# Optimization experiments

Measured on AMD Instinct MI355X. Metric: run time of the kernel, lower is better.

The kernel has to match this reference:

```python
import jax, jax.numpy as jnp
import numpy as np

NUM_HEADS = 16
HIDDEN = 1024
HEAD_DIM = HIDDEN // NUM_HEADS
B, L = 2, 2048


def setup_inputs() -> dict:
    key = jax.random.key(0)
    ks = jax.random.split(key, 5)
    scale = 1.0 / np.sqrt(HIDDEN)
    return {
        "x": jax.random.normal(ks[0], (B, L, HIDDEN), dtype=jnp.float32),
        "Wq": jax.random.normal(ks[1], (HIDDEN, HIDDEN), dtype=jnp.float32) * scale,
        "Wk": jax.random.normal(ks[2], (HIDDEN, HIDDEN), dtype=jnp.float32) * scale,
        "Wv": jax.random.normal(ks[3], (HIDDEN, HIDDEN), dtype=jnp.float32) * scale,
        "Wo": jax.random.normal(ks[4], (HIDDEN, HIDDEN), dtype=jnp.float32) * scale,
    }


def reference(x, Wq, Wk, Wv, Wo):
    b, l, _ = x.shape
    # projections (torch nn.Linear: y = x @ W.T), reshape to (B,L,H,D)
    q = (x @ Wq.T).reshape(b, l, NUM_HEADS, HEAD_DIM)
    k = (x @ Wk.T).reshape(b, l, NUM_HEADS, HEAD_DIM)
    v = (x @ Wv.T).reshape(b, l, NUM_HEADS, HEAD_DIM)
    # positive feature map
    q = jax.nn.elu(q) + 1.0
    k = jax.nn.elu(k) + 1.0
    # causal linear attention via cumulative kv outer products
    kv = jnp.einsum('blhd,blhe->blhde', k, v)          # (B,L,H,D,D)
    kv_cumsum = jnp.cumsum(kv, axis=1)
    k_cumsum = jnp.cumsum(k, axis=1)
    out = jnp.einsum('blhd,blhde->blhe', q, kv_cumsum)  # (B,L,H,D)
    normalizer = jnp.clip(jnp.einsum('blhd,blhd->blh', q, k_cumsum), 1e-6, None)
    out = out / normalizer[..., None]
    out = out.reshape(b, l, HIDDEN)
    return out @ Wo.T
```

## Files before the change

### kernel.cpp

```cpp
#include <hip/hip_runtime.h>
#include <cstdint>
#include <cstddef>

#define HID 1024
#define NH 16
#define HD 64
#define BB 2
#define LL 2048
#define MM (BB*LL)
#define CHUNK 64
#define NT (LL/CHUNK)
#define BHn (BB*NH)
#define SP 72

typedef __bf16 bf16;
typedef __attribute__((ext_vector_type(8))) __bf16 bf16x8;
typedef __attribute__((ext_vector_type(4))) float f32x4;

__device__ __forceinline__ f32x4 mfma16(bf16x8 a, bf16x8 b, f32x4 c){
  return __builtin_amdgcn_mfma_f32_16x16x32_bf16(a, b, c, 0, 0, 0);
}

__device__ __forceinline__ void gload16(const void* g, void* l){
  __builtin_amdgcn_global_load_lds(
      (const __attribute__((address_space(1))) unsigned int*)g,
      (__attribute__((address_space(3))) unsigned int*)l, 16, 0, 0);
}

__device__ __forceinline__ void barx(){
  asm volatile("" ::: "memory");
  __builtin_amdgcn_s_barrier();
  asm volatile("" ::: "memory");
}

#define WAITVM(N) asm volatile("s_waitcnt vmcnt(" #N ")" ::: "memory")

__global__ __launch_bounds__(256) void cast_all_k(
    const float* __restrict__ x,  const float* __restrict__ w0,
    const float* __restrict__ w1, const float* __restrict__ w2, const float* __restrict__ w3,
    bf16* __restrict__ xb, bf16* __restrict__ d0, bf16* __restrict__ d1,
    bf16* __restrict__ d2, bf16* __restrict__ d3)
{
  int bid = blockIdx.x;
  const float* s; bf16* d; int base;
  if (bid < 2048){ s = x; d = xb; base = bid; }
  else {
    int w = (bid - 2048) >> 9, r = (bid - 2048) & 511;
    s = (w==0)?w0:(w==1)?w1:(w==2)?w2:w3;
    d = (w==0)?d0:(w==1)?d1:(w==2)?d2:d3;
    base = r;
  }
  size_t i = (size_t)(base*256 + threadIdx.x) * 8;
  float4 v0 = *(const float4*)(s + i);
  float4 v1 = *(const float4*)(s + i + 4);
  union { bf16 h[8]; uint4 u; } pk;
  pk.h[0]=(bf16)v0.x; pk.h[1]=(bf16)v0.y; pk.h[2]=(bf16)v0.z; pk.h[3]=(bf16)v0.w;
  pk.h[4]=(bf16)v1.x; pk.h[5]=(bf16)v1.y; pk.h[6]=(bf16)v1.z; pk.h[7]=(bf16)v1.w;
  *(uint4*)(d + i) = pk.u;
}

template<int MODE>
__global__ __launch_bounds__(512, 2) void gemm8_k(
    const bf16* __restrict__ A,
    const bf16* __restrict__ W0, const bf16* __restrict__ W1, const bf16* __restrict__ W2,
    bf16* __restrict__ Qo, bf16* __restrict__ Kn, bf16* __restrict__ Vn,
    float* __restrict__ Outf)
{
  constexpr int NKT = HID/32;
  __shared__ bf16 lds[4][2][128*32];

  const int tid = threadIdx.x;
  const int wv = tid >> 6, lane = tid & 63;
  const int lrow = lane & 15, g4 = lane >> 4;
  const int wr = wv >> 2, wc = wv & 3;
  int bn = blockIdx.x, wsel = 0;
  const bf16* W = W0;
  if (MODE==0){ wsel = bn >> 3; bn &= 7; W = (wsel==0)?W0:((wsel==1)?W1:W2); }
  const int row0 = blockIdx.y*128, col0 = bn*128;

  const int sr = tid >> 2, sc = tid & 3;
  const int scs = sc ^ ((sr>>1)&3);
  const bf16* gA = A + (size_t)(row0 + sr)*HID + scs*8;
  const bf16* gB = W + (size_t)(col0 + sr)*HID + scs*8;
  const int ldst = tid*8;

  auto stage_tile = [&](int u){
    const int buf = u & 3;
    gload16(gA + u*32, (void*)&lds[buf][0][ldst]);
    gload16(gB + u*32, (void*)&lds[buf][1][ldst]);
  };

  const int koff = (g4 ^ ((lrow>>1)&3)) << 3;

  auto read_frags = [&](int u, bf16x8 (&fa)[4], bf16x8 (&fb)[2]){
    const int buf = u & 3;
    #pragma unroll
    for (int i=0;i<4;i++)
      fa[i] = *(const bf16x8*)&lds[buf][0][((wr*64 + i*16+lrow)<<5) + koff];
    #pragma unroll
    for (int j=0;j<2;j++)
      fb[j] = *(const bf16x8*)&lds[buf][1][((wc*32 + j*16+lrow)<<5) + koff];
  };

  f32x4 acc[4][2] = {};
  auto do_mfma = [&](bf16x8 (&fa)[4], bf16x8 (&fb)[2]){
    __builtin_amdgcn_s_setprio(1);
    #pragma unroll
    for (int i=0;i<4;i++)
      #pragma unroll
      for (int j=0;j<2;j++)
        acc[i][j] = mfma16(fa[i], fb[j], acc[i][j]);
    __builtin_amdgcn_s_setprio(0);
  };

  stage_tile(0); stage_tile(1); stage_tile(2);
  WAITVM(4);
  barx();
  bf16x8 fEa[4], fEb[2], fOa[4], fOb[2];
  read_frags(0, fEa, fEb);

  for (int t=0; t<NKT; t+=2){
    if (t+3 < NKT)      { stage_tile(t+3); WAITVM(4); }
    else if (t+3 == NKT){ WAITVM(2); }
    else                { WAITVM(0); }
    barx();
    read_frags(t+1, fOa, fOb);
    do_mfma(fEa, fEb);
    const int t2 = t+1;
    if (t2 < NKT-1){
      if (t2+3 < NKT)      { stage_tile(t2+3); WAITVM(4); }
      else if (t2+3 == NKT){ WAITVM(2); }
      else                 { WAITVM(0); }
      barx();
      read_frags(t2+1, fEa, fEb);
    }
    do_mfma(fOa, fOb);
  }

  #pragma unroll
  for (int i=0;i<4;i++){
    const int m0 = row0 + wr*64 + i*16 + g4*4;
    #pragma unroll
    for (int j=0;j<2;j++){
      const int c = col0 + wc*32 + j*16 + lrow;
      #pragma unroll
      for (int r=0;r<4;r++){
        float v = acc[i][j][r];
        if (MODE==1){
          Outf[(size_t)(m0+r)*HID + c] = v;
        } else {
          if (wsel<2) v = v>0.f ? v+1.f : __expf(v);
          bf16 bv = (bf16)v;
          if      (wsel==0) Qo[(size_t)(m0+r)*HID + c] = bv;
          else if (wsel==1) Kn[(size_t)(m0+r)*HID + c] = bv;
          else              Vn[(size_t)(m0+r)*HID + c] = bv;
        }
      }
    }
  }
}

__global__ __launch_bounds__(256) void pass1_k(const bf16* __restrict__ Kn, const bf16* __restrict__ Vn,
                                               float* __restrict__ SkvT, float* __restrict__ ksum)
{
  __shared__ bf16 KT[64*SP];
  __shared__ bf16 VT[64*SP];
  const int blk = blockIdx.x;
  const int bh = blk >> 5, t = blk & (NT-1);
  const int b = bh>>4, h = bh&15;
  const int tid = threadIdx.x;
  const int we = tid >> 6, lane = tid & 63;
  const int lrow = lane&15, g4 = lane>>4, lk8 = g4*8;
  const int sj = tid >> 2, c4 = tid & 3;
  const bf16* kb = Kn + ((size_t)(b*LL + t*CHUNK))*HID + h*HD;
  const bf16* vb = Vn + ((size_t)(b*LL + t*CHUNK))*HID + h*HD;

  {
    const bf16* ks = kb + (size_t)sj*HID + c4*16;
    const bf16* vs = vb + (size_t)sj*HID + c4*16;
    bf16x8 kr0 = *(const bf16x8*)&ks[0], kr1 = *(const bf16x8*)&ks[8];
    bf16x8 vr0 = *(const bf16x8*)&vs[0], vr1 = *(const bf16x8*)&vs[8];
    #pragma unroll
    for (int e=0;e<8;e++){
      KT[(c4*16+e)*SP + sj]   = kr0[e];
      KT[(c4*16+8+e)*SP + sj] = kr1[e];
      VT[(c4*16+e)*SP + sj]   = vr0[e];
      VT[(c4*16+8+e)*SP + sj] = vr1[e];
    }
  }
  __syncthreads();

  f32x4 acc[4] = {};
  #pragma unroll
  for (int kk=0;kk<2;kk++){
    bf16x8 fa = *(const bf16x8*)&VT[(we*16 + lrow)*SP + kk*32 + lk8];
    #pragma unroll
    for (int j=0;j<4;j++){
      bf16x8 fb = *(const bf16x8*)&KT[(j*16 + lrow)*SP + kk*32 + lk8];
      acc[j] = mfma16(fa, fb, acc[j]);
    }
  }
  float* so = SkvT + (size_t)blk*4096;
  #pragma unroll
  for (int j=0;j<4;j++)
    #pragma unroll
    for (int r=0;r<4;r++)
      so[(we*16 + g4*4 + r)*64 + j*16 + lrow] = acc[j][r];

  {
    const int row = we*16 + lrow;
    float s = 0.f;
    #pragma unroll
    for (int u=0;u<2;u++){
      bf16x8 k8 = *(const bf16x8*)&KT[row*SP + g4*16 + u*8];
      #pragma unroll
      for (int e=0;e<8;e++) s += (float)k8[e];
    }
    s += __shfl_xor(s,16); s += __shfl_xor(s,32);
    if (g4==0) ksum[(size_t)blk*64 + row] = s;
  }
}

__global__ __launch_bounds__(256) void pass2_k(const float* __restrict__ SkvT, const float* __restrict__ ksum,
                                               bf16* __restrict__ Sexcl, float* __restrict__ ksx)
{
  int gid = blockIdx.x*256 + threadIdx.x;
  if (gid < BHn*4096){
    int bh = gid >> 12, e = gid & 4095;
    float run = 0.f;
    size_t base = (size_t)bh*NT*4096 + e;
    #pragma unroll 4
    for (int t=0;t<NT;t++){
      Sexcl[base + (size_t)t*4096] = (bf16)run;
      run += SkvT[base + (size_t)t*4096];
    }
  } else if (gid < BHn*4096 + BHn*64){
    int g2 = gid - BHn*4096;
    int bh = g2 >> 6, d = g2 & 63;
    float run = 0.f;
    size_t base = (size_t)bh*NT*64 + d;
    #pragma unroll 4
    for (int t=0;t<NT;t++){
      ksx[base + (size_t)t*64] = run;
      run += ksum[base + (size_t)t*64];
    }
  }
}

__global__ __launch_bounds__(256) void pass3_k(const bf16* __restrict__ Q, const bf16* __restrict__ Kn,
                                               const bf16* __restrict__ Sexcl, const bf16* __restrict__ Vn,
                                               const float* __restrict__ ksx, bf16* __restrict__ Obuf)
{
  __shared__ bf16 P[64*SP];
  __shared__ bf16 VT[64*SP];
  const int blk = blockIdx.x;
  const int bh = blk>>5, t = blk&(NT-1);
  const int b = bh>>4, h = bh&15;
  const int tid = threadIdx.x;
  const int w = tid>>6, lane = tid&63;
  const int lrow = lane&15, g4 = lane>>4, lk8 = g4*8;
  const int sj = tid>>2, c4 = tid&3;
  const bf16* qb = Q  + ((size_t)(b*LL + t*CHUNK))*HID + h*HD;
  const bf16* kb = Kn + ((size_t)(b*LL + t*CHUNK))*HID + h*HD;
  const bf16* vb = Vn + ((size_t)(b*LL + t*CHUNK))*HID + h*HD;

  {
    const bf16* vs = vb + (size_t)sj*HID + c4*16;
    bf16x8 vr0 = *(const bf16x8*)&vs[0], vr1 = *(const bf16x8*)&vs[8];
    #pragma unroll
    for (int e=0;e<8;e++){
      VT[(c4*16+e)*SP + sj]   = vr0[e];
      VT[(c4*16+8+e)*SP + sj] = vr1[e];
    }
  }

  bf16x8 aq[2], bk[4][2];
  #pragma unroll
  for (int kk=0;kk<2;kk++){
    aq[kk] = *(const bf16x8*)&qb[(size_t)(w*16+lrow)*HID + kk*32 + lk8];
    #pragma unroll
    for (int j=0;j<4;j++)
      bk[j][kk] = *(const bf16x8*)&kb[(size_t)(j*16+lrow)*HID + kk*32 + lk8];
  }
  f32x4 sacc[4] = {};
  #pragma unroll
  for (int kk=0;kk<2;kk++)
    #pragma unroll
    for (int j=0;j<4;j++)
      sacc[j] = mfma16(aq[kk], bk[j][kk], sacc[j]);
  float rs[4];
  #pragma unroll
  for (int r=0;r<4;r++){
    int irow = w*16 + g4*4 + r;
    float p = 0.f;
    #pragma unroll
    for (int j=0;j<4;j++){
      int jcol = j*16 + lrow;
      float v = (jcol <= irow) ? sacc[j][r] : 0.f;
      sacc[j][r] = v;
      p += v;
    }
    p += __shfl_xor(p,1); p += __shfl_xor(p,2);
    p += __shfl_xor(p,4); p += __shfl_xor(p,8);
    rs[r] = p;
  }
  #pragma unroll
  for (int j=0;j<4;j++)
    #pragma unroll
    for (int r=0;r<4;r++)
      P[(w*16+g4*4+r)*SP + j*16+lrow] = (bf16)sacc[j][r];
  const float* kp = ksx + (size_t)blk*64;
  float zA;
  {
    float s = 0.f;
    #pragma unroll
    for (int kk=0;kk<2;kk++){
      const float* k8 = kp + kk*32 + lk8;
      bf16x8 q = aq[kk];
      #pragma unroll
      for (int j=0;j<8;j++) s += (float)q[j] * k8[j];
    }
    s += __shfl_xor(s,16); s += __shfl_xor(s,32);
    zA = s;
  }
  const bf16* sb = Sexcl + (size_t)blk*4096;
  f32x4 oacc[4] = {};
  #pragma unroll
  for (int kk=0;kk<2;kk++)
    #pragma unroll
    for (int j=0;j<4;j++){
      bf16x8 bs = *(const bf16x8*)&sb[(size_t)(j*16+lrow)*64 + kk*32 + lk8];
      oacc[j] = mfma16(aq[kk], bs, oacc[j]);
    }
  __syncthreads();
  #pragma unroll
  for (int kk=0;kk<2;kk++){
    bf16x8 ap = *(const bf16x8*)&P[(w*16+lrow)*SP + kk*32 + lk8];
    #pragma unroll
    for (int j=0;j<4;j++){
      bf16x8 bv = *(const bf16x8*)&VT[(j*16+lrow)*SP + kk*32 + lk8];
      oacc[j] = mfma16(ap, bv, oacc[j]);
    }
  }
  bf16* ob = Obuf + ((size_t)(b*LL + t*CHUNK))*HID + h*HD;
  #pragma unroll
  for (int r=0;r<4;r++){
    float z = __shfl(zA, g4*4 + r) + rs[r];
    z = fmaxf(z, 1e-6f);
    float inv = 1.0f/z;
    int irow = w*16 + g4*4 + r;
    #pragma unroll
    for (int j=0;j<4;j++)
      ob[(size_t)irow*HID + j*16+lrow] = (bf16)(oacc[j][r]*inv);
  }
}

extern "C" void kernel_launch(void* const* d_in, const int* in_sizes, int n_in,
                              void* d_out, int out_size, void* d_ws, size_t ws_size,
                              hipStream_t stream)
{
  const float* x  = (const float*)d_in[0];
  const float* Wq = (const float*)d_in[1];
  const float* Wk = (const float*)d_in[2];
  const float* Wv = (const float*)d_in[3];
  const float* Wo = (const float*)d_in[4];
  float* out = (float*)d_out;

  char* p = (char*)d_ws;
  auto alloc = [&](size_t bytes){ void* r = (void*)p; p += (bytes + 255) & ~(size_t)255; return r; };
  bf16* xb   = (bf16*)alloc((size_t)MM*HID*2);
  bf16* Wqb  = (bf16*)alloc((size_t)HID*HID*2);
  bf16* Wkb  = (bf16*)alloc((size_t)HID*HID*2);
  bf16* Wvb  = (bf16*)alloc((size_t)HID*HID*2);
  bf16* Wob  = (bf16*)alloc((size_t)HID*HID*2);
  bf16* Qb   = (bf16*)alloc((size_t)MM*HID*2);
  bf16* Knb  = (bf16*)alloc((size_t)MM*HID*2);
  bf16* Vnb  = (bf16*)alloc((size_t)MM*HID*2);
  bf16* Ob   = (bf16*)alloc((size_t)MM*HID*2);
  float* SkvT  = (float*)alloc((size_t)BHn*NT*4096*4);
  bf16*  Sexcl = (bf16*) alloc((size_t)BHn*NT*4096*2);
  float* ksum  = (float*)alloc((size_t)BHn*NT*64*4);
  float* ksx   = (float*)alloc((size_t)BHn*NT*64*4);

  cast_all_k<<<dim3(4096), 256, 0, stream>>>(x, Wq,Wk,Wv,Wo, xb, Wqb,Wkb,Wvb,Wob);
  gemm8_k<0><<<dim3(24,32), 512, 0, stream>>>(xb, Wqb,Wkb,Wvb, Qb,Knb,Vnb, nullptr);
  pass1_k<<<dim3(BHn*NT), 256, 0, stream>>>(Knb, Vnb, SkvT, ksum);
  pass2_k<<<dim3((BHn*4096 + BHn*64 + 255)/256), 256, 0, stream>>>(SkvT, ksum, Sexcl, ksx);
  pass3_k<<<dim3(BHn*NT), 256, 0, stream>>>(Qb, Knb, Sexcl, Vnb, ksx, Ob);
  gemm8_k<1><<<dim3(8,32), 512, 0, stream>>>(Ob, Wob,nullptr,nullptr, nullptr,nullptr,nullptr, out);
}
```

Baseline: 156.7 us.

## Group chunk pairs into segments for linear-attention state scan

Each block now handles a segment of two 64-row chunks instead of one. The per-segment KV state is summed in segsum, scanned over 16 segments rather than 32, and the attention kernel updates the running state inside the block between its two chunks. This halves the number of state matrices written, scanned and read through global memory. In exchange there are half as many blocks, serial work inside each block, and an extra bf16 rounding of the in-block state update.

```diff
diff --git a/kernel.cpp b/kernel.cpp
--- a/kernel.cpp
+++ b/kernel.cpp
@@ -10,6 +10,7 @@
 #define MM (BB*LL)
 #define CHUNK 64
 #define NT (LL/CHUNK)
+#define NSEG 16
 #define BHn (BB*NH)
 #define SP 72
 
@@ -160,198 +161,259 @@
   }
 }
 
-__global__ __launch_bounds__(256) void pass1_k(const bf16* __restrict__ Kn, const bf16* __restrict__ Vn,
-                                               float* __restrict__ SkvT, float* __restrict__ ksum)
+__global__ __launch_bounds__(256, 2) void segsum_k(const bf16* __restrict__ Kn, const bf16* __restrict__ Vn,
+                                                   float* __restrict__ Sseg, float* __restrict__ kseg)
 {
   __shared__ bf16 KT[64*SP];
   __shared__ bf16 VT[64*SP];
-  const int blk = blockIdx.x;
-  const int bh = blk >> 5, t = blk & (NT-1);
+  const int bx = blockIdx.x;
+  const int bh = bx >> 4, seg = bx & (NSEG-1);
   const int b = bh>>4, h = bh&15;
   const int tid = threadIdx.x;
   const int we = tid >> 6, lane = tid & 63;
   const int lrow = lane&15, g4 = lane>>4, lk8 = g4*8;
   const int sj = tid >> 2, c4 = tid & 3;
-  const bf16* kb = Kn + ((size_t)(b*LL + t*CHUNK))*HID + h*HD;
-  const bf16* vb = Vn + ((size_t)(b*LL + t*CHUNK))*HID + h*HD;
-
-  {
-    const bf16* ks = kb + (size_t)sj*HID + c4*16;
-    const bf16* vs = vb + (size_t)sj*HID + c4*16;
-    bf16x8 kr0 = *(const bf16x8*)&ks[0], kr1 = *(const bf16x8*)&ks[8];
-    bf16x8 vr0 = *(const bf16x8*)&vs[0], vr1 = *(const bf16x8*)&vs[8];
-    #pragma unroll
-    for (int e=0;e<8;e++){
-      KT[(c4*16+e)*SP + sj]   = kr0[e];
-      KT[(c4*16+8+e)*SP + sj] = kr1[e];
-      VT[(c4*16+e)*SP + sj]   = vr0[e];
-      VT[(c4*16+8+e)*SP + sj] = vr1[e];
-    }
-  }
-  __syncthreads();
 
   f32x4 acc[4] = {};
+  float krow = 0.f;
+
   #pragma unroll
-  for (int kk=0;kk<2;kk++){
-    bf16x8 fa = *(const bf16x8*)&VT[(we*16 + lrow)*SP + kk*32 + lk8];
-    #pragma unroll
-    for (int j=0;j<4;j++){
-      bf16x8 fb = *(const bf16x8*)&KT[(j*16 + lrow)*SP + kk*32 + lk8];
-      acc[j] = mfma16(fa, fb, acc[j]);
-    }
-  }
-  float* so = SkvT + (size_t)blk*4096;
+  for (int c=0;c<2;c++){
+    const int cg = seg*2 + c;
+    const bf16* kb = Kn + ((size_t)(b*LL + cg*CHUNK))*HID + h*HD;
+    const bf16* vb = Vn + ((size_t)(b*LL + cg*CHUNK))*HID + h*HD;
+    {
+      const bf16* ks = kb + (size_t)sj*HID + c4*16;
+      const bf16* vs = vb + (size_t)sj*HID + c4*16;
+      bf16x8 kr0 = *(const bf16x8*)&ks[0], kr1 = *(const bf16x8*)&ks[8];
+      bf16x8 vr0 = *(const bf16x8*)&vs[0], vr1 = *(const bf16x8*)&vs[8];
+      #pragma unroll
+      for (int e=0;e<8;e++){
+        KT[(c4*16+e)*SP + sj]   = kr0[e];
+        KT[(c4*16+8+e)*SP + sj] = kr1[e];
+        VT[(c4*16+e)*SP + sj]   = vr0[e];
+        VT[(c4*16+8+e)*SP + sj] = vr1[e];
+      }
+    }
+    __syncthreads();
+    #pragma unroll
+    for (int kk=0;kk<2;kk++){
+      bf16x8 fa = *(const bf16x8*)&VT[(we*16 + lrow)*SP + kk*32 + lk8];
+      #pragma unroll
+      for (int j=0;j<4;j++){
+        bf16x8 fb = *(const bf16x8*)&KT[(j*16 + lrow)*SP + kk*32 + lk8];
+        acc[j] = mfma16(fa, fb, acc[j]);
+      }
+    }
+    {
+      const int row = we*16 + lrow;
+      float s = 0.f;
+      #pragma unroll
+      for (int u=0;u<2;u++){
+        bf16x8 k8 = *(const bf16x8*)&KT[row*SP + g4*16 + u*8];
+        #pragma unroll
+        for (int e=0;e<8;e++) s += (float)k8[e];
+      }
+      s += __shfl_xor(s,16); s += __shfl_xor(s,32);
+      krow += s;
+    }
+    __syncthreads();
+  }
+
+  float* so = Sseg + (size_t)bx*4096;
   #pragma unroll
   for (int j=0;j<4;j++)
     #pragma unroll
     for (int r=0;r<4;r++)
       so[(we*16 + g4*4 + r)*64 + j*16 + lrow] = acc[j][r];
-
-  {
-    const int row = we*16 + lrow;
-    float s = 0.f;
-    #pragma unroll
-    for (int u=0;u<2;u++){
-      bf16x8 k8 = *(const bf16x8*)&KT[row*SP + g4*16 + u*8];
-      #pragma unroll
-      for (int e=0;e<8;e++) s += (float)k8[e];
-    }
-    s += __shfl_xor(s,16); s += __shfl_xor(s,32);
-    if (g4==0) ksum[(size_t)blk*64 + row] = s;
-  }
-}
-
-__global__ __launch_bounds__(256) void pass2_k(const float* __restrict__ SkvT, const float* __restrict__ ksum,
-                                               bf16* __restrict__ Sexcl, float* __restrict__ ksx)
+  if (g4==0) kseg[(size_t)bx*64 + we*16 + lrow] = krow;
+}
+
+__global__ __launch_bounds__(256) void segscan_k(const float* __restrict__ Sseg, const float* __restrict__ kseg,
+                                                 bf16* __restrict__ Sexb, float* __restrict__ ksxb)
 {
   int gid = blockIdx.x*256 + threadIdx.x;
   if (gid < BHn*4096){
     int bh = gid >> 12, e = gid & 4095;
     float run = 0.f;
-    size_t base = (size_t)bh*NT*4096 + e;
+    size_t base = (size_t)bh*NSEG*4096 + e;
     #pragma unroll 4
-    for (int t=0;t<NT;t++){
-      Sexcl[base + (size_t)t*4096] = (bf16)run;
-      run += SkvT[base + (size_t)t*4096];
+    for (int s=0;s<NSEG;s++){
+      Sexb[base + (size_t)s*4096] = (bf16)run;
+      run += Sseg[base + (size_t)s*4096];
     }
   } else if (gid < BHn*4096 + BHn*64){
     int g2 = gid - BHn*4096;
     int bh = g2 >> 6, d = g2 & 63;
     float run = 0.f;
-    size_t base = (size_t)bh*NT*64 + d;
+    size_t base = (size_t)bh*NSEG*64 + d;
     #pragma unroll 4
-    for (int t=0;t<NT;t++){
-      ksx[base + (size_t)t*64] = run;
-      run += ksum[base + (size_t)t*64];
-    }
-  }
-}
-
-__global__ __launch_bounds__(256) void pass3_k(const bf16* __restrict__ Q, const bf16* __restrict__ Kn,
-                                               const bf16* __restrict__ Sexcl, const bf16* __restrict__ Vn,
-                                               const float* __restrict__ ksx, bf16* __restrict__ Obuf)
-{
-  __shared__ bf16 P[64*SP];
+    for (int s=0;s<NSEG;s++){
+      ksxb[base + (size_t)s*64] = run;
+      run += kseg[base + (size_t)s*64];
+    }
+  }
+}
+
+__global__ __launch_bounds__(256, 2) void attn_k(const bf16* __restrict__ Q, const bf16* __restrict__ Kn,
+                                                 const bf16* __restrict__ Vn, const bf16* __restrict__ Sexb,
+                                                 const float* __restrict__ ksxb, bf16* __restrict__ Obuf)
+{
+  __shared__ bf16 KT[64*SP];
   __shared__ bf16 VT[64*SP];
-  const int blk = blockIdx.x;
-  const int bh = blk>>5, t = blk&(NT-1);
+  __shared__ bf16 P [64*SP];
+  __shared__ bf16 Sm[64*SP];
+  __shared__ float ksum_lds[64];
+  const int bx = blockIdx.x;
+  const int bh = bx >> 4, seg = bx & (NSEG-1);
   const int b = bh>>4, h = bh&15;
   const int tid = threadIdx.x;
-  const int w = tid>>6, lane = tid&63;
+  const int w = tid >> 6, lane = tid & 63;
   const int lrow = lane&15, g4 = lane>>4, lk8 = g4*8;
-  const int sj = tid>>2, c4 = tid&3;
-  const bf16* qb = Q  + ((size_t)(b*LL + t*CHUNK))*HID + h*HD;
-  const bf16* kb = Kn + ((size_t)(b*LL + t*CHUNK))*HID + h*HD;
-  const bf16* vb = Vn + ((size_t)(b*LL + t*CHUNK))*HID + h*HD;
-
+  const int sj = tid >> 2, c4 = tid & 3;
+
+  if (tid < 64) ksum_lds[tid] = ksxb[(size_t)bx*64 + tid];
   {
-    const bf16* vs = vb + (size_t)sj*HID + c4*16;
-    bf16x8 vr0 = *(const bf16x8*)&vs[0], vr1 = *(const bf16x8*)&vs[8];
-    #pragma unroll
-    for (int e=0;e<8;e++){
-      VT[(c4*16+e)*SP + sj]   = vr0[e];
-      VT[(c4*16+8+e)*SP + sj] = vr1[e];
-    }
-  }
-
-  bf16x8 aq[2], bk[4][2];
-  #pragma unroll
-  for (int kk=0;kk<2;kk++){
-    aq[kk] = *(const bf16x8*)&qb[(size_t)(w*16+lrow)*HID + kk*32 + lk8];
-    #pragma unroll
-    for (int j=0;j<4;j++)
-      bk[j][kk] = *(const bf16x8*)&kb[(size_t)(j*16+lrow)*HID + kk*32 + lk8];
-  }
-  f32x4 sacc[4] = {};
-  #pragma unroll
-  for (int kk=0;kk<2;kk++)
-    #pragma unroll
-    for (int j=0;j<4;j++)
-      sacc[j] = mfma16(aq[kk], bk[j][kk], sacc[j]);
-  float rs[4];
-  #pragma unroll
-  for (int r=0;r<4;r++){
-    int irow = w*16 + g4*4 + r;
-    float p = 0.f;
-    #pragma unroll
-    for (int j=0;j<4;j++){
-      int jcol = j*16 + lrow;
-      float v = (jcol <= irow) ? sacc[j][r] : 0.f;
-      sacc[j][r] = v;
-      p += v;
-    }
-    p += __shfl_xor(p,1); p += __shfl_xor(p,2);
-    p += __shfl_xor(p,4); p += __shfl_xor(p,8);
-    rs[r] = p;
-  }
+    const bf16* sp = Sexb + (size_t)bx*4096 + tid*16;
+    bf16x8 s0 = *(const bf16x8*)&sp[0], s1 = *(const bf16x8*)&sp[8];
+    const int e = tid>>2, d0 = (tid&3)*16;
+    *(bf16x8*)&Sm[e*SP + d0]     = s0;
+    *(bf16x8*)&Sm[e*SP + d0 + 8] = s1;
+  }
+  __syncthreads();
+  f32x4 Srun[4];
   #pragma unroll
   for (int j=0;j<4;j++)
     #pragma unroll
     for (int r=0;r<4;r++)
-      P[(w*16+g4*4+r)*SP + j*16+lrow] = (bf16)sacc[j][r];
-  const float* kp = ksx + (size_t)blk*64;
-  float zA;
-  {
-    float s = 0.f;
+      Srun[j][r] = (float)Sm[(w*16+g4*4+r)*SP + j*16+lrow];
+
+  #pragma unroll
+  for (int c=0;c<2;c++){
+    const int cg = seg*2 + c;
+    const bf16* kb = Kn + ((size_t)(b*LL + cg*CHUNK))*HID + h*HD;
+    const bf16* vb = Vn + ((size_t)(b*LL + cg*CHUNK))*HID + h*HD;
+    const bf16* qb = Q  + ((size_t)(b*LL + cg*CHUNK))*HID + h*HD;
+    {
+      const bf16* ks = kb + (size_t)sj*HID + c4*16;
+      const bf16* vs = vb + (size_t)sj*HID + c4*16;
+      bf16x8 kr0 = *(const bf16x8*)&ks[0], kr1 = *(const bf16x8*)&ks[8];
+      bf16x8 vr0 = *(const bf16x8*)&vs[0], vr1 = *(const bf16x8*)&vs[8];
+      #pragma unroll
+      for (int e=0;e<8;e++){
+        KT[(c4*16+e)*SP + sj]   = kr0[e];
+        KT[(c4*16+8+e)*SP + sj] = kr1[e];
+        VT[(c4*16+e)*SP + sj]   = vr0[e];
+        VT[(c4*16+8+e)*SP + sj] = vr1[e];
+      }
+    }
+    bf16x8 aq[2], bk[4][2];
     #pragma unroll
     for (int kk=0;kk<2;kk++){
-      const float* k8 = kp + kk*32 + lk8;
-      bf16x8 q = aq[kk];
-      #pragma unroll
-      for (int j=0;j<8;j++) s += (float)q[j] * k8[j];
-    }
-    s += __shfl_xor(s,16); s += __shfl_xor(s,32);
-    zA = s;
-  }
-  const bf16* sb = Sexcl + (size_t)blk*4096;
-  f32x4 oacc[4] = {};
-  #pragma unroll
-  for (int kk=0;kk<2;kk++)
-    #pragma unroll
-    for (int j=0;j<4;j++){
-      bf16x8 bs = *(const bf16x8*)&sb[(size_t)(j*16+lrow)*64 + kk*32 + lk8];
-      oacc[j] = mfma16(aq[kk], bs, oacc[j]);
-    }
-  __syncthreads();
-  #pragma unroll
-  for (int kk=0;kk<2;kk++){
-    bf16x8 ap = *(const bf16x8*)&P[(w*16+lrow)*SP + kk*32 + lk8];
-    #pragma unroll
-    for (int j=0;j<4;j++){
-      bf16x8 bv = *(const bf16x8*)&VT[(j*16+lrow)*SP + kk*32 + lk8];
-      oacc[j] = mfma16(ap, bv, oacc[j]);
-    }
-  }
-  bf16* ob = Obuf + ((size_t)(b*LL + t*CHUNK))*HID + h*HD;
-  #pragma unroll
-  for (int r=0;r<4;r++){
-    float z = __shfl(zA, g4*4 + r) + rs[r];
-    z = fmaxf(z, 1e-6f);
-    float inv = 1.0f/z;
-    int irow = w*16 + g4*4 + r;
+      aq[kk] = *(const bf16x8*)&qb[(size_t)(w*16+lrow)*HID + kk*32 + lk8];
+      #pragma unroll
+      for (int j=0;j<4;j++)
+        bk[j][kk] = *(const bf16x8*)&kb[(size_t)(j*16+lrow)*HID + kk*32 + lk8];
+    }
+    __syncthreads();
+    f32x4 sacc[4] = {};
+    #pragma unroll
+    for (int kk=0;kk<2;kk++)
+      #pragma unroll
+      for (int j=0;j<4;j++)
+        sacc[j] = mfma16(aq[kk], bk[j][kk], sacc[j]);
+    float rs[4];
+    #pragma unroll
+    for (int r=0;r<4;r++){
+      int irow = w*16 + g4*4 + r;
+      float p = 0.f;
+      #pragma unroll
+      for (int j=0;j<4;j++){
+        int jcol = j*16 + lrow;
+        float v = (jcol <= irow) ? sacc[j][r] : 0.f;
+        sacc[j][r] = v;
+        p += v;
+      }
+      p += __shfl_xor(p,1); p += __shfl_xor(p,2);
+      p += __shfl_xor(p,4); p += __shfl_xor(p,8);
+      rs[r] = p;
+    }
+    float zA;
+    {
+      float s = 0.f;
+      #pragma unroll
+      for (int kk=0;kk<2;kk++){
+        const float* k8 = ksum_lds + kk*32 + lk8;
+        bf16x8 q = aq[kk];
+        #pragma unroll
+        for (int j=0;j<8;j++) s += (float)q[j] * k8[j];
+      }
+      s += __shfl_xor(s,16); s += __shfl_xor(s,32);
+      zA = s;
+    }
+    f32x4 oacc[4] = {};
+    #pragma unroll
+    for (int kk=0;kk<2;kk++)
+      #pragma unroll
+      for (int j=0;j<4;j++){
+        bf16x8 bs = *(const bf16x8*)&Sm[(j*16+lrow)*SP + kk*32 + lk8];
+        oacc[j] = mfma16(aq[kk], bs, oacc[j]);
+      }
     #pragma unroll
     for (int j=0;j<4;j++)
-      ob[(size_t)irow*HID + j*16+lrow] = (bf16)(oacc[j][r]*inv);
+      #pragma unroll
+      for (int r=0;r<4;r++)
+        P[(w*16+g4*4+r)*SP + j*16+lrow] = (bf16)sacc[j][r];
+    __syncthreads();
+    #pragma unroll
+    for (int kk=0;kk<2;kk++){
+      bf16x8 ap = *(const bf16x8*)&P[(w*16+lrow)*SP + kk*32 + lk8];
+      #pragma unroll
+      for (int j=0;j<4;j++){
+        bf16x8 bv = *(const bf16x8*)&VT[(j*16+lrow)*SP + kk*32 + lk8];
+        oacc[j] = mfma16(ap, bv, oacc[j]);
+      }
+    }
+    bf16* ob = Obuf + ((size_t)(b*LL + cg*CHUNK))*HID + h*HD;
+    #pragma unroll
+    for (int r=0;r<4;r++){
+      float z = __shfl(zA, g4*4 + r) + rs[r];
+      z = fmaxf(z, 1e-6f);
+      float inv = 1.0f/z;
+      int irow = w*16 + g4*4 + r;
+      #pragma unroll
+      for (int j=0;j<4;j++)
+        ob[(size_t)irow*HID + j*16+lrow] = (bf16)(oacc[j][r]*inv);
+    }
+    if (c==0){
+      #pragma unroll
+      for (int kk=0;kk<2;kk++){
+        bf16x8 fa = *(const bf16x8*)&VT[(w*16+lrow)*SP + kk*32 + lk8];
+        #pragma unroll
+        for (int j=0;j<4;j++){
+          bf16x8 fb = *(const bf16x8*)&KT[(j*16+lrow)*SP + kk*32 + lk8];
+          Srun[j] = mfma16(fa, fb, Srun[j]);
+        }
+      }
+      {
+        const int row = w*16 + lrow;
+        float s = 0.f;
+        #pragma unroll
+        for (int u=0;u<2;u++){
+          bf16x8 k8 = *(const bf16x8*)&KT[row*SP + g4*16 + u*8];
+          #pragma unroll
+          for (int e=0;e<8;e++) s += (float)k8[e];
+        }
+        s += __shfl_xor(s,16); s += __shfl_xor(s,32);
+        if (g4==0) ksum_lds[row] += s;
+      }
+      #pragma unroll
+      for (int j=0;j<4;j++)
+        #pragma unroll
+        for (int r=0;r<4;r++)
+          Sm[(w*16+g4*4+r)*SP + j*16+lrow] = (bf16)Srun[j][r];
+    }
+    __syncthreads();
   }
 }
 
@@ -377,15 +439,15 @@
   bf16* Knb  = (bf16*)alloc((size_t)MM*HID*2);
   bf16* Vnb  = (bf16*)alloc((size_t)MM*HID*2);
   bf16* Ob   = (bf16*)alloc((size_t)MM*HID*2);
-  float* SkvT  = (float*)alloc((size_t)BHn*NT*4096*4);
-  bf16*  Sexcl = (bf16*) alloc((size_t)BHn*NT*4096*2);
-  float* ksum  = (float*)alloc((size_t)BHn*NT*64*4);
-  float* ksx   = (float*)alloc((size_t)BHn*NT*64*4);
+  float* Sseg = (float*)alloc((size_t)BHn*NSEG*4096*4);
+  bf16*  Sexb = (bf16*) alloc((size_t)BHn*NSEG*4096*2);
+  float* kseg = (float*)alloc((size_t)BHn*NSEG*64*4);
+  float* ksxb = (float*)alloc((size_t)BHn*NSEG*64*4);
 
   cast_all_k<<<dim3(4096), 256, 0, stream>>>(x, Wq,Wk,Wv,Wo, xb, Wqb,Wkb,Wvb,Wob);
   gemm8_k<0><<<dim3(24,32), 512, 0, stream>>>(xb, Wqb,Wkb,Wvb, Qb,Knb,Vnb, nullptr);
-  pass1_k<<<dim3(BHn*NT), 256, 0, stream>>>(Knb, Vnb, SkvT, ksum);
-  pass2_k<<<dim3((BHn*4096 + BHn*64 + 255)/256), 256, 0, stream>>>(SkvT, ksum, Sexcl, ksx);
-  pass3_k<<<dim3(BHn*NT), 256, 0, stream>>>(Qb, Knb, Sexcl, Vnb, ksx, Ob);
+  segsum_k<<<dim3(BHn*NSEG), 256, 0, stream>>>(Knb, Vnb, Sseg, kseg);
+  segscan_k<<<dim3((BHn*4096 + BHn*64 + 255)/256), 256, 0, stream>>>(Sseg, kseg, Sexb, ksxb);
+  attn_k<<<dim3(BHn*NSEG), 256, 0, stream>>>(Qb, Knb, Vnb, Sexb, ksxb, Ob);
   gemm8_k<1><<<dim3(8,32), 512, 0, stream>>>(Ob, Wob,nullptr,nullptr, nullptr,nullptr,nullptr, out);
 }
```

Result: faster. 150.4 us (-4.0%).
